# Kernel optimization log

Measured on AMD Instinct MI355X. Metric: run time of the kernel, lower is better.

## Reference

```python
import jax, jax.numpy as jnp
import numpy as np

N = 50000        # total nodes across batch
K = 16           # max neighbors per node (padded with index 0)
E = 800000       # directed edges / messages
B = 1024         # molecules
MAXM = 48        # max nodes per molecule (padded with index 0)
FEATURE_FDIM = 9
ALL_FDIM = 10    # feature_dist_graph (9) + reshaped rij distance (1)
H = 64           # hidden_dim
NUM_ITERS = 2
NEG_INF = -1e9


def setup_inputs() -> dict:
    key = jax.random.key(0)
    ks = jax.random.split(key, 16)
    s = 1.0 / np.sqrt(H)
    return {
        "target_features": jax.random.normal(ks[0], (N, FEATURE_FDIM), jnp.float32),
        "feature_dist_graph": jax.random.normal(ks[1], (E, ALL_FDIM - 1), jnp.float32),
        "rij_dist_pairs": jax.random.uniform(ks[2], (E,), jnp.float32),
        "start_end_env": jax.random.randint(ks[3], (N, K), 0, N + 1),
        "b_scope": jax.random.randint(ks[4], (N, K), 0, E),
        "l_scope": jax.random.randint(ks[5], (B, MAXM), 0, N + 1),
        "scope_update": jax.random.randint(ks[6], (E,), 0, N + 1),
        "scope_update_lig": jax.random.randint(ks[7], (E,), 0, N + 1),
        "W_emb": jax.random.uniform(ks[8], (FEATURE_FDIM, H), jnp.float32, 0.1, 0.9),
        "b_emb": jnp.zeros((H,), jnp.float32),
        "W_dist": jax.random.uniform(ks[9], (ALL_FDIM, H), jnp.float32, 0.1, 0.9),
        "b_dist": jnp.zeros((H,), jnp.float32),
        "W_gat": jax.random.normal(ks[10], (H, H), jnp.float32) * s,
        "Wm_gat": jax.random.normal(ks[11], (H, H), jnp.float32) * s,
        "a_gat": jax.random.normal(ks[12], (2 * H,), jnp.float32) * s,
    }


def reference(target_features, feature_dist_graph, rij_dist_pairs,
              start_end_env, b_scope, l_scope, scope_update, scope_update_lig,
              W_emb, b_emb, W_dist, b_dist, W_gat, Wm_gat, a_gat):
    # node embedding over origin features
    h = target_features @ W_emb + b_emb                        # [N, H]
    # edge message embedding over pair features + distance
    msg_in = jnp.concatenate([feature_dist_graph, rij_dist_pairs[:, None]], axis=1)
    message = msg_in @ W_dist + b_dist                         # [E, H]
    # prepend zero pad row (index 0 = padding for ragged gathers)
    hp = jnp.concatenate([jnp.zeros((1, H), h.dtype), h], axis=0)  # [N+1, H]
    pad_mask = (start_end_env == 0)                            # [N, K]
    upd_mask = (scope_update_lig > 0).astype(h.dtype)[:, None]  # [E, 1]
    for _ in range(NUM_ITERS):
        nb = hp[start_end_env]                                 # [N, K, H] gather neighbors
        mg = message[b_scope]                                  # [N, K, H] gather messages
        Wn = nb @ W_gat                                        # [N, K, H]
        Wm = mg @ Wm_gat                                       # [N, K, H]
        # GAT attention logits: leaky_relu(a^T [Wn || Wm])
        logits = jax.nn.leaky_relu(
            jnp.einsum('nkh,h->nk', Wn, a_gat[:H]) +
            jnp.einsum('nkh,h->nk', Wm, a_gat[H:]), 0.2)       # [N, K]
        logits = jnp.where(pad_mask, NEG_INF, logits)
        alpha = jax.nn.softmax(logits, axis=1)                 # [N, K]
        new_h = jax.nn.elu(jnp.einsum('nk,nkh->nh', alpha, Wn + Wm))  # [N, H]
        hp = jnp.concatenate([jnp.zeros((1, H), new_h.dtype), new_h], axis=0)
        # scatter updated node features back into edge messages
        message = hp[scope_update] * upd_mask                  # [E, H]
    cmp_enc = hp[l_scope]                                      # [B, MAXM, H]
    return cmp_enc.sum(axis=1)                                 # [B, H]
```

## Files before the change

### kernel.cpp

```cpp
#include <hip/hip_runtime.h>
#include <hip/hip_bf16.h>

#define N_NODES 50000
#define K_NB 16
#define E_EDGES 800000
#define B_MOL 1024
#define MAXM_M 48
#define FDIM 9
#define ADIM 10
#define H 64
#define NEG_INF_F (-1e9f)
#define PRE_NODE_BLOCKS 196
#define EDGE_BLOCKS 3125

typedef __bf16 bf16x8 __attribute__((ext_vector_type(8)));
typedef float f32x4 __attribute__((ext_vector_type(4)));

__device__ inline float readlane_f(float v, int l) {
    return __int_as_float(__builtin_amdgcn_readlane(__float_as_int(v), l));
}
__device__ inline int readlane_i(int v, int l) {
    return __builtin_amdgcn_readlane(v, l);
}
__device__ inline float bf2f(unsigned u) {
    return __uint_as_float(u << 16);
}
__device__ inline unsigned short f2bf(float f) {
    unsigned x = __float_as_uint(f);
    return (unsigned short)((x + 0x7fffu + ((x >> 16) & 1u)) >> 16);
}

#define GLOAD_U16(dst, voff, sbase) \
    asm volatile("global_load_ushort %0, %1, %2" : "=v"(dst) : "v"(voff), "s"(sbase))
#define GLOAD_F32(dst, voff, sbase) \
    asm volatile("global_load_dword %0, %1, %2" : "=v"(dst) : "v"(voff), "s"(sbase))

#define DRAIN16(a) \
    asm volatile("s_waitcnt vmcnt(0)" \
        : "+v"(a[0]), "+v"(a[1]), "+v"(a[2]), "+v"(a[3]), \
          "+v"(a[4]), "+v"(a[5]), "+v"(a[6]), "+v"(a[7]), \
          "+v"(a[8]), "+v"(a[9]), "+v"(a[10]), "+v"(a[11]), \
          "+v"(a[12]), "+v"(a[13]), "+v"(a[14]), "+v"(a[15]))
#define HOLD16(a) \
    asm volatile("" \
        : "+v"(a[0]), "+v"(a[1]), "+v"(a[2]), "+v"(a[3]), \
          "+v"(a[4]), "+v"(a[5]), "+v"(a[6]), "+v"(a[7]), \
          "+v"(a[8]), "+v"(a[9]), "+v"(a[10]), "+v"(a[11]), \
          "+v"(a[12]), "+v"(a[13]), "+v"(a[14]), "+v"(a[15]))

__global__ __launch_bounds__(256) void k_fold(
    const float* __restrict__ W_emb, const float* __restrict__ b_emb,
    const float* __restrict__ W_dist, const float* __restrict__ b_dist,
    const float* __restrict__ W_gat, const float* __restrict__ Wm_gat,
    const float* __restrict__ a_gat,
    float* __restrict__ W2, float* __restrict__ c2,
    float* __restrict__ W3, float* __restrict__ c3,
    float* __restrict__ wa, float* __restrict__ ca,
    float* __restrict__ va, float* __restrict__ vb,
    float* __restrict__ wv9, float* __restrict__ cv,
    unsigned short* __restrict__ WintT)
{
    __shared__ float s_va[64], s_vb[64];
    int tid = threadIdx.x;
    int h = tid & 63, g = tid >> 6;
    if (g == 0) {
        float acc = 0.f;
        for (int t = 0; t < H; ++t) acc += W_gat[h * H + t] * a_gat[t];
        s_va[h] = acc; va[h] = acc;
    } else if (g == 1) {
        float acc = 0.f;
        for (int t = 0; t < H; ++t) acc += Wm_gat[h * H + t] * a_gat[H + t];
        s_vb[h] = acc; vb[h] = acc;
    } else if (g == 2) {
        float acc = 0.f;
        for (int t = 0; t < H; ++t) acc += b_dist[t] * Wm_gat[t * H + h];
        c2[h] = acc;
    } else {
        float acc = 0.f;
        for (int t = 0; t < H; ++t) acc += b_emb[t] * W_gat[t * H + h];
        c3[h] = acc;
    }
    __syncthreads();
    for (int q = tid; q < 640; q += 256) {
        int j = q >> 6, hh = q & 63;
        float acc = 0.f;
        for (int t = 0; t < H; ++t) acc += W_dist[j * H + t] * Wm_gat[t * H + hh];
        W2[q] = acc;
    }
    for (int q = tid; q < 576; q += 256) {
        int j = q >> 6, hh = q & 63;
        float acc = 0.f;
        for (int t = 0; t < H; ++t) acc += W_emb[j * H + t] * W_gat[t * H + hh];
        W3[q] = acc;
    }
    for (int q = tid; q < H * 2 * H; q += 256) {
        int n = q >> 7, k = q & 127;
        float v = (k & 1) ? Wm_gat[(k >> 1) * H + n] : W_gat[(k >> 1) * H + n];
        WintT[q] = f2bf(v);
    }
    if (tid < ADIM) {
        float acc = 0.f;
        for (int t = 0; t < H; ++t) acc += W_dist[tid * H + t] * s_vb[t];
        wa[tid] = acc;
    } else if (tid == ADIM) {
        float acc = 0.f;
        for (int t = 0; t < H; ++t) acc += b_dist[t] * s_vb[t];
        ca[0] = acc;
    } else if (tid >= 16 && tid < 16 + FDIM) {
        int j = tid - 16;
        float acc = 0.f;
        for (int t = 0; t < H; ++t) acc += W_emb[j * H + t] * s_va[t];
        wv9[j] = acc;
    } else if (tid == 31) {
        float acc = 0.f;
        for (int t = 0; t < H; ++t) acc += b_emb[t] * s_va[t];
        cv[0] = acc;
    }
}

__global__ __launch_bounds__(256) void k_pre(
    const float* __restrict__ tf, const float* __restrict__ fdg,
    const float* __restrict__ rij,
    const int* __restrict__ su, const int* __restrict__ sul,
    const float* __restrict__ wa, const float* __restrict__ ca,
    const float* __restrict__ wv9, const float* __restrict__ cv,
    float* __restrict__ t1A, unsigned short* __restrict__ tfp,
    unsigned short* __restrict__ emsg, int* __restrict__ sue)
{
    int bid = blockIdx.x;
    if (bid < PRE_NODE_BLOCKS) {
        int n = bid * 256 + threadIdx.x;
        if (n == 0) {
            t1A[0] = 0.f;
            uint4 z = make_uint4(0, 0, 0, 0);
            ((uint4*)tfp)[0] = z; ((uint4*)tfp)[1] = z;
        }
        if (n >= N_NODES) return;
        float f[FDIM];
        float acc = cv[0];
#pragma unroll
        for (int j = 0; j < FDIM; ++j) {
            f[j] = tf[n * FDIM + j];
            acc += f[j] * wv9[j];
        }
        t1A[n + 1] = acc;
        unsigned rec[8];
#pragma unroll
        for (int j = 0; j < 4; ++j)
            rec[j] = (unsigned)f2bf(f[2 * j]) | ((unsigned)f2bf(f[2 * j + 1]) << 16);
        rec[4] = (unsigned)f2bf(f[8]);
        rec[5] = 0; rec[6] = 0; rec[7] = 0;
        uint4* dst = (uint4*)(tfp + (size_t)(n + 1) * 16);
        dst[0] = make_uint4(rec[0], rec[1], rec[2], rec[3]);
        dst[1] = make_uint4(rec[4], rec[5], rec[6], rec[7]);
    } else {
        int e = (bid - PRE_NODE_BLOCKS) * 256 + threadIdx.x;
        float f[ADIM];
#pragma unroll
        for (int j = 0; j < FDIM; ++j) f[j] = fdg[(size_t)e * FDIM + j];
        f[FDIM] = rij[e];
        float acc = ca[0];
#pragma unroll
        for (int j = 0; j < ADIM; ++j) acc += f[j] * wa[j];
        unsigned rec[8];
#pragma unroll
        for (int j = 0; j < 5; ++j)
            rec[j] = (unsigned)f2bf(f[2 * j]) | ((unsigned)f2bf(f[2 * j + 1]) << 16);
        rec[5] = __float_as_uint(acc);
        rec[6] = 0; rec[7] = 0;
        uint4* dst = (uint4*)(emsg + (size_t)e * 16);
        dst[0] = make_uint4(rec[0], rec[1], rec[2], rec[3]);
        dst[1] = make_uint4(rec[4], rec[5], rec[6], rec[7]);
        sue[e] = (sul[e] > 0) ? su[e] : 0;
    }
}

__global__ __launch_bounds__(256) void k_gat1(
    const int* __restrict__ sse, const int* __restrict__ bsc,
    const float* __restrict__ t1A, const unsigned short* __restrict__ tfp,
    const unsigned short* __restrict__ emsg,
    const float* __restrict__ W2, const float* __restrict__ c2,
    const float* __restrict__ W3, const float* __restrict__ c3,
    const float* __restrict__ va, const float* __restrict__ vb,
    unsigned short* __restrict__ hp2bf, float* __restrict__ t1B,
    float* __restrict__ t2B)
{
    int wave = threadIdx.x >> 6;
    int lane = threadIdx.x & 63;
    int n = blockIdx.x * 4 + wave;
    if (n == 0) {
        hp2bf[lane] = 0;
        if (lane == 0) { t1B[0] = 0.f; t2B[0] = 0.f; }
    }
    if (n >= N_NODES) return;

    int kidx = 0, ke = 0;
    float lg = NEG_INF_F;
    if (lane < K_NB) {
        kidx = sse[n * K_NB + lane];
        ke   = bsc[n * K_NB + lane];
        float g2 = __uint_as_float(*(const unsigned*)(emsg + (size_t)ke * 16 + 10));
        float p = t1A[kidx] + g2;
        p = (p > 0.f) ? p : 0.2f * p;
        lg = (kidx == 0) ? NEG_INF_F : p;
    }

    unsigned wn_u[K_NB], wm_u[K_NB];
    int offr = (lane & 15) * 2;
#pragma unroll
    for (int k = 0; k < K_NB; ++k) {
        const unsigned short* pk = tfp + (size_t)readlane_i(kidx, k) * 16;
        GLOAD_U16(wn_u[k], offr, pk);
    }
#pragma unroll
    for (int k = 0; k < K_NB; ++k) {
        const unsigned short* pe = emsg + (size_t)readlane_i(ke, k) * 16;
        GLOAD_U16(wm_u[k], offr, pe);
    }

    float m = lg;
#pragma unroll
    for (int o = 8; o > 0; o >>= 1) m = fmaxf(m, __shfl_xor(m, o, 64));
    float ex = __expf(lg - m);
    float s = ex;
#pragma unroll
    for (int o = 8; o > 0; o >>= 1) s += __shfl_xor(s, o, 64);
    float alpha = ex / s;

    DRAIN16(wn_u);
    HOLD16(wm_u);

    float fr = 0.f, frm = 0.f, beta = 0.f;
#pragma unroll
    for (int k = 0; k < K_NB; ++k) {
        float ak = readlane_f(alpha, k);
        fr  += ak * bf2f(wn_u[k]);
        frm += ak * bf2f(wm_u[k]);
        beta += (readlane_i(kidx, k) > 0) ? ak : 0.f;
    }
    float acc = c2[lane] + beta * c3[lane];
#pragma unroll
    for (int j = 0; j < FDIM; ++j) acc += readlane_f(fr, j) * W3[j * H + lane];
#pragma unroll
    for (int j = 0; j < ADIM; ++j) acc += readlane_f(frm, j) * W2[j * H + lane];
    float o = (acc > 0.f) ? acc : expm1f(acc);
    hp2bf[(size_t)(n + 1) * H + lane] = f2bf(o);
    float ta = o * va[lane], tb = o * vb[lane];
#pragma unroll
    for (int q = 32; q > 0; q >>= 1) {
        ta += __shfl_xor(ta, q, 64);
        tb += __shfl_xor(tb, q, 64);
    }
    if (lane == 0) { t1B[n + 1] = ta; t2B[n + 1] = tb; }
}

__global__ __launch_bounds__(1024) void k_gat2(
    const int* __restrict__ sse, const int* __restrict__ bsc,
    const int* __restrict__ sue,
    const float* __restrict__ t1B, const float* __restrict__ t2B,
    const unsigned short* __restrict__ hp2bf,
    const unsigned short* __restrict__ WintT,
    float* __restrict__ hp3)
{
    __shared__ unsigned s_rows[16][72];
    int wave = threadIdx.x >> 6;
    int lane = threadIdx.x & 63;
    int row  = blockIdx.x * 16 + wave;
    int n    = row - 1;

    float gn = 0.f, gm = 0.f;
    if (n >= 0 && n < N_NODES) {
        int kidx = 0, ksu = 0;
        float lg = NEG_INF_F;
        if (lane < K_NB) {
            kidx = sse[n * K_NB + lane];
            int ke = bsc[n * K_NB + lane];
            ksu = sue[ke];
            float p = t1B[kidx] + t2B[ksu];
            p = (p > 0.f) ? p : 0.2f * p;
            lg = (kidx == 0) ? NEG_INF_F : p;
        }

        unsigned wn_u[K_NB], wm_u[K_NB];
        int off = lane * 2;
#pragma unroll
        for (int k = 0; k < K_NB; ++k) {
            const unsigned short* pk = hp2bf + (size_t)readlane_i(kidx, k) * H;
            GLOAD_U16(wn_u[k], off, pk);
        }
#pragma unroll
        for (int k = 0; k < K_NB; ++k) {
            const unsigned short* ps = hp2bf + (size_t)readlane_i(ksu, k) * H;
            GLOAD_U16(wm_u[k], off, ps);
        }

        float m = lg;
#pragma unroll
        for (int o = 8; o > 0; o >>= 1) m = fmaxf(m, __shfl_xor(m, o, 64));
        float ex = __expf(lg - m);
        float s = ex;
#pragma unroll
        for (int o = 8; o > 0; o >>= 1) s += __shfl_xor(s, o, 64);
        float alpha = ex / s;

        DRAIN16(wn_u);
        HOLD16(wm_u);

#pragma unroll
        for (int k = 0; k < K_NB; ++k) {
            float ak = readlane_f(alpha, k);
            gn += ak * bf2f(wn_u[k]);
            gm += ak * bf2f(wm_u[k]);
        }
    }
    s_rows[wave][lane] = (unsigned)f2bf(gn) | ((unsigned)f2bf(gm) << 16);
    __syncthreads();

    if (wave < 4) {
        int t = wave;
        int m = lane & 15, q = lane >> 4;
        union UB { uint4 u; bf16x8 v; };
        bf16x8 bfr[4];
        const unsigned short* bp = WintT + (size_t)(t * 16 + m) * 128 + q * 8;
#pragma unroll
        for (int kk = 0; kk < 4; ++kk) {
            UB ub; ub.u = *(const uint4*)(bp + kk * 32);
            bfr[kk] = ub.v;
        }
        f32x4 acc = (f32x4){0.f, 0.f, 0.f, 0.f};
#pragma unroll
        for (int kk = 0; kk < 4; ++kk) {
            UB ua; ua.u = *(const uint4*)&s_rows[m][kk * 16 + q * 4];
            acc = __builtin_amdgcn_mfma_f32_16x16x32_bf16(ua.v, bfr[kk], acc, 0, 0, 0);
        }
        int row0 = blockIdx.x * 16;
#pragma unroll
        for (int r = 0; r < 4; ++r) {
            int rr = row0 + q * 4 + r;
            if (rr <= N_NODES) {
                float v = acc[r];
                hp3[(size_t)rr * H + t * 16 + m] = (v > 0.f) ? v : expm1f(v);
            }
        }
    }
}

__global__ __launch_bounds__(256) void k_out(
    const int* __restrict__ l_scope, const float* __restrict__ hp,
    float* __restrict__ out)
{
    int wave = threadIdx.x >> 6;
    int lane = threadIdx.x & 63;
    int b = blockIdx.x * 4 + wave;
    if (b >= B_MOL) return;
    int idx48 = (lane < MAXM_M) ? l_scope[b * MAXM_M + lane] : 0;
    float v[MAXM_M];
    int off = lane * 4;
#pragma unroll
    for (int m = 0; m < MAXM_M; ++m) {
        const float* pm = hp + (size_t)readlane_i(idx48, m) * H;
        GLOAD_F32(v[m], off, pm);
    }
    asm volatile("s_waitcnt vmcnt(0)"
        : "+v"(v[0]), "+v"(v[1]), "+v"(v[2]), "+v"(v[3]),
          "+v"(v[4]), "+v"(v[5]), "+v"(v[6]), "+v"(v[7]),
          "+v"(v[8]), "+v"(v[9]), "+v"(v[10]), "+v"(v[11]),
          "+v"(v[12]), "+v"(v[13]), "+v"(v[14]), "+v"(v[15]));
    asm volatile(""
        : "+v"(v[16]), "+v"(v[17]), "+v"(v[18]), "+v"(v[19]),
          "+v"(v[20]), "+v"(v[21]), "+v"(v[22]), "+v"(v[23]),
          "+v"(v[24]), "+v"(v[25]), "+v"(v[26]), "+v"(v[27]),
          "+v"(v[28]), "+v"(v[29]), "+v"(v[30]), "+v"(v[31]));
    asm volatile(""
        : "+v"(v[32]), "+v"(v[33]), "+v"(v[34]), "+v"(v[35]),
          "+v"(v[36]), "+v"(v[37]), "+v"(v[38]), "+v"(v[39]),
          "+v"(v[40]), "+v"(v[41]), "+v"(v[42]), "+v"(v[43]),
          "+v"(v[44]), "+v"(v[45]), "+v"(v[46]), "+v"(v[47]));
    float acc = 0.f;
#pragma unroll
    for (int m = 0; m < MAXM_M; ++m) acc += v[m];
    out[b * H + lane] = acc;
}

extern "C" void kernel_launch(void* const* d_in, const int* in_sizes, int n_in,
                              void* d_out, int out_size, void* d_ws, size_t ws_size,
                              hipStream_t stream)
{
    const float* tf     = (const float*)d_in[0];
    const float* fdg    = (const float*)d_in[1];
    const float* rij    = (const float*)d_in[2];
    const int*   sse    = (const int*)d_in[3];
    const int*   bsc    = (const int*)d_in[4];
    const int*   lsc    = (const int*)d_in[5];
    const int*   su     = (const int*)d_in[6];
    const int*   sul    = (const int*)d_in[7];
    const float* W_emb  = (const float*)d_in[8];
    const float* b_emb  = (const float*)d_in[9];
    const float* W_dist = (const float*)d_in[10];
    const float* b_dist = (const float*)d_in[11];
    const float* W_gat  = (const float*)d_in[12];
    const float* Wm_gat = (const float*)d_in[13];
    const float* a_gat  = (const float*)d_in[14];
    float* out = (float*)d_out;

    char* base = (char*)d_ws;
    size_t off = 0;
    auto alloc = [&](size_t bytes) {
        char* p = base + off;
        off = (off + bytes + 255) & ~(size_t)255;
        return p;
    };
    float* W2   = (float*)alloc(640 * 4);
    float* c2   = (float*)alloc(64 * 4);
    float* W3   = (float*)alloc(640 * 4);
    float* c3   = (float*)alloc(64 * 4);
    float* wa   = (float*)alloc(16 * 4);
    float* ca   = (float*)alloc(16 * 4);
    float* va   = (float*)alloc(64 * 4);
    float* vb   = (float*)alloc(64 * 4);
    float* wv9  = (float*)alloc(16 * 4);
    float* cv   = (float*)alloc(16 * 4);
    unsigned short* WintT = (unsigned short*)alloc(64 * 128 * 2);
    float* t1A  = (float*)alloc((size_t)(N_NODES + 1) * 4);
    float* t1B  = (float*)alloc((size_t)(N_NODES + 1) * 4);
    float* t2B  = (float*)alloc((size_t)(N_NODES + 1) * 4);
    int*   sue  = (int*)alloc((size_t)E_EDGES * 4);
    unsigned short* tfp   = (unsigned short*)alloc((size_t)(N_NODES + 1) * 16 * 2);
    unsigned short* hp2bf = (unsigned short*)alloc((size_t)(N_NODES + 1) * H * 2);
    char* big = alloc((size_t)E_EDGES * 32);
    unsigned short* emsg = (unsigned short*)big;
    float* hp3 = (float*)big;

    k_fold<<<dim3(1), dim3(256), 0, stream>>>(
        W_emb, b_emb, W_dist, b_dist, W_gat, Wm_gat, a_gat,
        W2, c2, W3, c3, wa, ca, va, vb, wv9, cv, WintT);

    k_pre<<<dim3(PRE_NODE_BLOCKS + EDGE_BLOCKS), dim3(256), 0, stream>>>(
        tf, fdg, rij, su, sul, wa, ca, wv9, cv, t1A, tfp, emsg, sue);

    k_gat1<<<dim3((N_NODES + 3) / 4), dim3(256), 0, stream>>>(
        sse, bsc, t1A, tfp, emsg, W2, c2, W3, c3, va, vb, hp2bf, t1B, t2B);

    k_gat2<<<dim3((N_NODES + 16) / 16), dim3(1024), 0, stream>>>(
        sse, bsc, sue, t1B, t2B, hp2bf, WintT, hp3);

    k_out<<<dim3(B_MOL / 4), dim3(256), 0, stream>>>(lsc, hp3, out);
}
```

Before: 208.4 us.

## Replace scalar first GAT projection with MFMA over folded bf16 weights

The first GAT iteration kernel now handles 16 rows per 1024-thread block. Per-wave aggregated features (fr, frm, beta and a bias indicator) are staged in shared memory, and one bf16 MFMA against a concatenated folded weight matrix (WcatT) produces the 64-wide output. A second MFMA against a va/vb matrix computes the next iteration's attention terms t1B/t2B, replacing the 19 readlane FMAs and cross-lane shuffle reductions per lane. This cuts per-node scalar work and reads of the fp32 weights, but adds block barriers, quantises the folded weights and the va/vb vectors to bf16, and drops the explicit zeroing of padding row 0 in favour of the computed row.

```diff
diff --git a/kernel.cpp b/kernel.cpp
--- a/kernel.cpp
+++ b/kernel.cpp
@@ -15,6 +15,7 @@
 
 typedef __bf16 bf16x8 __attribute__((ext_vector_type(8)));
 typedef float f32x4 __attribute__((ext_vector_type(4)));
+union UB { uint4 u; bf16x8 v; };
 
 __device__ inline float readlane_f(float v, int l) {
     return __int_as_float(__builtin_amdgcn_readlane(__float_as_int(v), l));
@@ -53,12 +54,10 @@
     const float* __restrict__ W_dist, const float* __restrict__ b_dist,
     const float* __restrict__ W_gat, const float* __restrict__ Wm_gat,
     const float* __restrict__ a_gat,
-    float* __restrict__ W2, float* __restrict__ c2,
-    float* __restrict__ W3, float* __restrict__ c3,
     float* __restrict__ wa, float* __restrict__ ca,
-    float* __restrict__ va, float* __restrict__ vb,
     float* __restrict__ wv9, float* __restrict__ cv,
-    unsigned short* __restrict__ WintT)
+    unsigned short* __restrict__ WintT, unsigned short* __restrict__ WcatT,
+    unsigned short* __restrict__ vabT)
 {
     __shared__ float s_va[64], s_vb[64];
     int tid = threadIdx.x;
@@ -66,37 +65,36 @@
     if (g == 0) {
         float acc = 0.f;
         for (int t = 0; t < H; ++t) acc += W_gat[h * H + t] * a_gat[t];
-        s_va[h] = acc; va[h] = acc;
+        s_va[h] = acc;
     } else if (g == 1) {
         float acc = 0.f;
         for (int t = 0; t < H; ++t) acc += Wm_gat[h * H + t] * a_gat[H + t];
-        s_vb[h] = acc; vb[h] = acc;
-    } else if (g == 2) {
-        float acc = 0.f;
-        for (int t = 0; t < H; ++t) acc += b_dist[t] * Wm_gat[t * H + h];
-        c2[h] = acc;
-    } else {
-        float acc = 0.f;
-        for (int t = 0; t < H; ++t) acc += b_emb[t] * W_gat[t * H + h];
-        c3[h] = acc;
+        s_vb[h] = acc;
     }
     __syncthreads();
-    for (int q = tid; q < 640; q += 256) {
-        int j = q >> 6, hh = q & 63;
-        float acc = 0.f;
-        for (int t = 0; t < H; ++t) acc += W_dist[j * H + t] * Wm_gat[t * H + hh];
-        W2[q] = acc;
-    }
-    for (int q = tid; q < 576; q += 256) {
-        int j = q >> 6, hh = q & 63;
-        float acc = 0.f;
-        for (int t = 0; t < H; ++t) acc += W_emb[j * H + t] * W_gat[t * H + hh];
-        W3[q] = acc;
-    }
     for (int q = tid; q < H * 2 * H; q += 256) {
         int n = q >> 7, k = q & 127;
         float v = (k & 1) ? Wm_gat[(k >> 1) * H + n] : W_gat[(k >> 1) * H + n];
         WintT[q] = f2bf(v);
+    }
+    for (int q = tid; q < 64 * 32; q += 256) {
+        int n = q >> 5, k = q & 31;
+        float acc = 0.f;
+        if (k < 9) {
+            for (int t = 0; t < H; ++t) acc += W_emb[k * H + t] * W_gat[t * H + n];
+        } else if (k < 19) {
+            for (int t = 0; t < H; ++t) acc += W_dist[(k - 9) * H + t] * Wm_gat[t * H + n];
+        } else if (k == 19) {
+            for (int t = 0; t < H; ++t) acc += b_emb[t] * W_gat[t * H + n];
+        } else if (k == 20) {
+            for (int t = 0; t < H; ++t) acc += b_dist[t] * Wm_gat[t * H + n];
+        }
+        WcatT[q] = f2bf(acc);
+    }
+    for (int q = tid; q < 16 * 64; q += 256) {
+        int n = q >> 6, k = q & 63;
+        float v = (n == 0) ? s_va[k] : (n == 1) ? s_vb[k] : 0.f;
+        vabT[q] = f2bf(v);
     }
     if (tid < ADIM) {
         float acc = 0.f;
@@ -175,83 +173,111 @@
     }
 }
 
-__global__ __launch_bounds__(256) void k_gat1(
+__global__ __launch_bounds__(1024) void k_gat1(
     const int* __restrict__ sse, const int* __restrict__ bsc,
     const float* __restrict__ t1A, const unsigned short* __restrict__ tfp,
     const unsigned short* __restrict__ emsg,
-    const float* __restrict__ W2, const float* __restrict__ c2,
-    const float* __restrict__ W3, const float* __restrict__ c3,
-    const float* __restrict__ va, const float* __restrict__ vb,
+    const unsigned short* __restrict__ WcatT,
+    const unsigned short* __restrict__ vabT,
     unsigned short* __restrict__ hp2bf, float* __restrict__ t1B,
     float* __restrict__ t2B)
 {
+    __shared__ __align__(16) unsigned short s_a[16][40];
+    __shared__ __align__(16) unsigned short s_o[16][72];
     int wave = threadIdx.x >> 6;
     int lane = threadIdx.x & 63;
-    int n = blockIdx.x * 4 + wave;
-    if (n == 0) {
-        hp2bf[lane] = 0;
-        if (lane == 0) { t1B[0] = 0.f; t2B[0] = 0.f; }
-    }
-    if (n >= N_NODES) return;
-
-    int kidx = 0, ke = 0;
-    float lg = NEG_INF_F;
-    if (lane < K_NB) {
-        kidx = sse[n * K_NB + lane];
-        ke   = bsc[n * K_NB + lane];
-        float g2 = __uint_as_float(*(const unsigned*)(emsg + (size_t)ke * 16 + 10));
-        float p = t1A[kidx] + g2;
-        p = (p > 0.f) ? p : 0.2f * p;
-        lg = (kidx == 0) ? NEG_INF_F : p;
-    }
-
-    unsigned wn_u[K_NB], wm_u[K_NB];
-    int offr = (lane & 15) * 2;
-#pragma unroll
-    for (int k = 0; k < K_NB; ++k) {
-        const unsigned short* pk = tfp + (size_t)readlane_i(kidx, k) * 16;
-        GLOAD_U16(wn_u[k], offr, pk);
-    }
-#pragma unroll
-    for (int k = 0; k < K_NB; ++k) {
-        const unsigned short* pe = emsg + (size_t)readlane_i(ke, k) * 16;
-        GLOAD_U16(wm_u[k], offr, pe);
-    }
-
-    float m = lg;
-#pragma unroll
-    for (int o = 8; o > 0; o >>= 1) m = fmaxf(m, __shfl_xor(m, o, 64));
-    float ex = __expf(lg - m);
-    float s = ex;
-#pragma unroll
-    for (int o = 8; o > 0; o >>= 1) s += __shfl_xor(s, o, 64);
-    float alpha = ex / s;
-
-    DRAIN16(wn_u);
-    HOLD16(wm_u);
+    int row0 = blockIdx.x * 16;
+    int row  = row0 + wave;
+    int n    = row - 1;
 
     float fr = 0.f, frm = 0.f, beta = 0.f;
-#pragma unroll
-    for (int k = 0; k < K_NB; ++k) {
-        float ak = readlane_f(alpha, k);
-        fr  += ak * bf2f(wn_u[k]);
-        frm += ak * bf2f(wm_u[k]);
-        beta += (readlane_i(kidx, k) > 0) ? ak : 0.f;
-    }
-    float acc = c2[lane] + beta * c3[lane];
-#pragma unroll
-    for (int j = 0; j < FDIM; ++j) acc += readlane_f(fr, j) * W3[j * H + lane];
-#pragma unroll
-    for (int j = 0; j < ADIM; ++j) acc += readlane_f(frm, j) * W2[j * H + lane];
-    float o = (acc > 0.f) ? acc : expm1f(acc);
-    hp2bf[(size_t)(n + 1) * H + lane] = f2bf(o);
-    float ta = o * va[lane], tb = o * vb[lane];
-#pragma unroll
-    for (int q = 32; q > 0; q >>= 1) {
-        ta += __shfl_xor(ta, q, 64);
-        tb += __shfl_xor(tb, q, 64);
-    }
-    if (lane == 0) { t1B[n + 1] = ta; t2B[n + 1] = tb; }
+    if (n >= 0 && n < N_NODES) {
+        int kidx = 0, ke = 0;
+        float lg = NEG_INF_F;
+        if (lane < K_NB) {
+            kidx = sse[n * K_NB + lane];
+            ke   = bsc[n * K_NB + lane];
+            float g2 = __uint_as_float(*(const unsigned*)(emsg + (size_t)ke * 16 + 10));
+            float p = t1A[kidx] + g2;
+            p = (p > 0.f) ? p : 0.2f * p;
+            lg = (kidx == 0) ? NEG_INF_F : p;
+        }
+        unsigned wn_u[K_NB], wm_u[K_NB];
+        int offr = (lane & 15) * 2;
+#pragma unroll
+        for (int k = 0; k < K_NB; ++k) {
+            const unsigned short* pk = tfp + (size_t)readlane_i(kidx, k) * 16;
+            GLOAD_U16(wn_u[k], offr, pk);
+        }
+#pragma unroll
+        for (int k = 0; k < K_NB; ++k) {
+            const unsigned short* pe = emsg + (size_t)readlane_i(ke, k) * 16;
+            GLOAD_U16(wm_u[k], offr, pe);
+        }
+        float m = lg;
+#pragma unroll
+        for (int o = 8; o > 0; o >>= 1) m = fmaxf(m, __shfl_xor(m, o, 64));
+        float ex = __expf(lg - m);
+        float s = ex;
+#pragma unroll
+        for (int o = 8; o > 0; o >>= 1) s += __shfl_xor(s, o, 64);
+        float alpha = ex / s;
+
+        DRAIN16(wn_u);
+        HOLD16(wm_u);
+#pragma unroll
+        for (int k = 0; k < K_NB; ++k) {
+            float ak = readlane_f(alpha, k);
+            fr  += ak * bf2f(wn_u[k]);
+            frm += ak * bf2f(wm_u[k]);
+            beta += (readlane_i(kidx, k) > 0) ? ak : 0.f;
+        }
+    }
+    if (lane < FDIM)  s_a[wave][lane] = f2bf(fr);
+    if (lane < ADIM)  s_a[wave][FDIM + lane] = f2bf(frm);
+    if (lane == 10)   s_a[wave][19] = f2bf(beta);
+    if (lane == 11)   s_a[wave][20] = (row == 0) ? 0 : (unsigned short)0x3F80;
+    if (lane >= 21 && lane < 32) s_a[wave][lane] = 0;
+    __syncthreads();
+
+    int m16 = lane & 15, q = lane >> 4;
+    if (wave < 4) {
+        int t = wave;
+        UB ub; ub.u = *(const uint4*)(WcatT + (size_t)(t * 16 + m16) * 32 + q * 8);
+        UB ua; ua.u = *(const uint4*)&s_a[m16][q * 8];
+        f32x4 acc = (f32x4){0.f, 0.f, 0.f, 0.f};
+        acc = __builtin_amdgcn_mfma_f32_16x16x32_bf16(ua.v, ub.v, acc, 0, 0, 0);
+#pragma unroll
+        for (int r = 0; r < 4; ++r) {
+            int rr = row0 + q * 4 + r;
+            float v = acc[r];
+            float o = (v > 0.f) ? v : expm1f(v);
+            unsigned short ob = f2bf(o);
+            s_o[q * 4 + r][t * 16 + m16] = ob;
+            if (rr <= N_NODES) hp2bf[(size_t)rr * H + t * 16 + m16] = ob;
+        }
+    }
+    __syncthreads();
+    if (wave == 0) {
+        UB a0, a1, b0, b1;
+        a0.u = *(const uint4*)&s_o[m16][q * 8];
+        a1.u = *(const uint4*)&s_o[m16][32 + q * 8];
+        b0.u = *(const uint4*)(vabT + (size_t)m16 * 64 + q * 8);
+        b1.u = *(const uint4*)(vabT + (size_t)m16 * 64 + 32 + q * 8);
+        f32x4 acc = (f32x4){0.f, 0.f, 0.f, 0.f};
+        acc = __builtin_amdgcn_mfma_f32_16x16x32_bf16(a0.v, b0.v, acc, 0, 0, 0);
+        acc = __builtin_amdgcn_mfma_f32_16x16x32_bf16(a1.v, b1.v, acc, 0, 0, 0);
+        if (m16 < 2) {
+#pragma unroll
+            for (int r = 0; r < 4; ++r) {
+                int rr = row0 + q * 4 + r;
+                if (rr <= N_NODES) {
+                    if (m16 == 0) t1B[rr] = acc[r];
+                    else          t2B[rr] = acc[r];
+                }
+            }
+        }
+    }
 }
 
 __global__ __launch_bounds__(1024) void k_gat2(
@@ -262,7 +288,7 @@
     const unsigned short* __restrict__ WintT,
     float* __restrict__ hp3)
 {
-    __shared__ unsigned s_rows[16][72];
+    __shared__ __align__(16) unsigned s_rows[16][72];
     int wave = threadIdx.x >> 6;
     int lane = threadIdx.x & 63;
     int row  = blockIdx.x * 16 + wave;
@@ -280,7 +306,6 @@
             p = (p > 0.f) ? p : 0.2f * p;
             lg = (kidx == 0) ? NEG_INF_F : p;
         }
-
         unsigned wn_u[K_NB], wm_u[K_NB];
         int off = lane * 2;
 #pragma unroll
@@ -293,7 +318,6 @@
             const unsigned short* ps = hp2bf + (size_t)readlane_i(ksu, k) * H;
             GLOAD_U16(wm_u[k], off, ps);
         }
-
         float m = lg;
 #pragma unroll
         for (int o = 8; o > 0; o >>= 1) m = fmaxf(m, __shfl_xor(m, o, 64));
@@ -305,7 +329,6 @@
 
         DRAIN16(wn_u);
         HOLD16(wm_u);
-
 #pragma unroll
         for (int k = 0; k < K_NB; ++k) {
             float ak = readlane_f(alpha, k);
@@ -319,7 +342,6 @@
     if (wave < 4) {
         int t = wave;
         int m = lane & 15, q = lane >> 4;
-        union UB { uint4 u; bf16x8 v; };
         bf16x8 bfr[4];
         const unsigned short* bp = WintT + (size_t)(t * 16 + m) * 128 + q * 8;
 #pragma unroll
@@ -410,17 +432,13 @@
         off = (off + bytes + 255) & ~(size_t)255;
         return p;
     };
-    float* W2   = (float*)alloc(640 * 4);
-    float* c2   = (float*)alloc(64 * 4);
-    float* W3   = (float*)alloc(640 * 4);
-    float* c3   = (float*)alloc(64 * 4);
     float* wa   = (float*)alloc(16 * 4);
     float* ca   = (float*)alloc(16 * 4);
-    float* va   = (float*)alloc(64 * 4);
-    float* vb   = (float*)alloc(64 * 4);
     float* wv9  = (float*)alloc(16 * 4);
     float* cv   = (float*)alloc(16 * 4);
     unsigned short* WintT = (unsigned short*)alloc(64 * 128 * 2);
+    unsigned short* WcatT = (unsigned short*)alloc(64 * 32 * 2);
+    unsigned short* vabT  = (unsigned short*)alloc(16 * 64 * 2);
     float* t1A  = (float*)alloc((size_t)(N_NODES + 1) * 4);
     float* t1B  = (float*)alloc((size_t)(N_NODES + 1) * 4);
     float* t2B  = (float*)alloc((size_t)(N_NODES + 1) * 4);
@@ -433,13 +451,13 @@
 
     k_fold<<<dim3(1), dim3(256), 0, stream>>>(
         W_emb, b_emb, W_dist, b_dist, W_gat, Wm_gat, a_gat,
-        W2, c2, W3, c3, wa, ca, va, vb, wv9, cv, WintT);
+        wa, ca, wv9, cv, WintT, WcatT, vabT);
 
     k_pre<<<dim3(PRE_NODE_BLOCKS + EDGE_BLOCKS), dim3(256), 0, stream>>>(
         tf, fdg, rij, su, sul, wa, ca, wv9, cv, t1A, tfp, emsg, sue);
 
-    k_gat1<<<dim3((N_NODES + 3) / 4), dim3(256), 0, stream>>>(
-        sse, bsc, t1A, tfp, emsg, W2, c2, W3, c3, va, vb, hp2bf, t1B, t2B);
+    k_gat1<<<dim3((N_NODES + 16) / 16), dim3(1024), 0, stream>>>(
+        sse, bsc, t1A, tfp, emsg, WcatT, vabT, hp2bf, t1B, t2B);
 
     k_gat2<<<dim3((N_NODES + 16) / 16), dim3(1024), 0, stream>>>(
         sse, bsc, sue, t1B, t2B, hp2bf, WintT, hp3);
```

Measured after the change: 240.5 us. 15.4% more time.
